# Kernel tuning notes

Hardware: AMD Instinct MI355X
Metric: run time of the kernel (lower is better)

Reference implementation:

```python
import jax, jax.numpy as jnp
import numpy as np

SELECTOR = jnp.array([29, 49, 79])
N_FINAL = 6
N_EM_ITERS = 10
LOG_2PI = float(np.log(2.0 * np.pi))


def _logdet2(c):
    # log determinant of trailing 2x2 matrices
    return jnp.log(c[..., 0, 0] * c[..., 1, 1] - c[..., 0, 1] * c[..., 1, 0])


def _inv2(c):
    # analytic inverse of trailing 2x2 matrices
    det = c[..., 0, 0] * c[..., 1, 1] - c[..., 0, 1] * c[..., 1, 0]
    inv = jnp.stack([
        jnp.stack([c[..., 1, 1], -c[..., 0, 1]], axis=-1),
        jnp.stack([-c[..., 1, 0], c[..., 0, 0]], axis=-1),
    ], axis=-2)
    return inv / det[..., None, None]


def _initial_state(probas, trajectories):
    B, M = probas.shape
    tsel = trajectories[:, :, SELECTOR, :]                       # [B,M,3,2]
    dots = jnp.einsum('bmtd,bntd->btmn', tsel, tsel)             # [B,3,M,M]
    d1 = jnp.einsum('bmtd,bmtd->btm', tsel, tsel)                # [B,3,M]
    R = jnp.sqrt(d1[:, :, :, None] + d1[:, :, None, :] - 2.0 * dots)
    thr = jnp.quantile(R[:, -1].reshape(B, -1), 0.15, axis=-1)[:, None, None, None]
    adj = (R <= thr).astype(probas.dtype).prod(axis=1)           # [B,M,M]
    worked = jnp.ones((B, M), dtype=probas.dtype)
    bidx = jnp.arange(B)
    idxs = []
    for _ in range(N_FINAL):
        score = (adj * probas[:, None, :]).sum(axis=2) * worked  # [B,M]
        amax = jnp.argmax(score, axis=-1)                        # [B]
        worked = worked * (1.0 - adj[bidx, amax])
        idxs.append(amax)
    return jnp.stack(idxs, axis=1)                               # [B,6]


def _coefficients(cov6, trajectories, traj6, probas6):
    cov6_sel = cov6[:, :, SELECTOR]                              # [B,6,3,2,2]
    prec = _inv2(cov6_sel)                                       # [B,6,3,2,2]
    diff = traj6[:, :, SELECTOR][:, :, None] - trajectories[:, :, SELECTOR][:, None]  # [B,6,M,3,2]
    qform = jnp.einsum('bnmti,bntij,bnmtj->bnmt', diff, prec, diff)
    logdet = _logdet2(cov6_sel)[:, :, None, :]                   # [B,6,1,3]
    pM = jnp.exp((-LOG_2PI - 0.5 * logdet - 0.5 * qform).sum(axis=-1)) + 1e-8  # [B,6,M]
    num = pM * probas6[:, :, None]
    return num / (num.sum(axis=1, keepdims=True) + 1e-8)


def _forward(non_normalized_probas, trajectories, covariance_matrices):
    B = trajectories.shape[0]
    probas = jax.nn.softmax(non_normalized_probas, axis=-1)
    idx = jax.lax.stop_gradient(_initial_state(probas, trajectories))  # [B,6]
    b = jnp.arange(B)[:, None]
    traj6 = trajectories[b, idx]                                 # [B,6,T,2]
    probas6 = jax.nn.softmax(jnp.take_along_axis(non_normalized_probas, idx, axis=1), axis=-1)
    cov6 = covariance_matrices[b, idx]                           # [B,6,T,2,2]
    for _ in range(N_EM_ITERS):
        pM = jax.lax.stop_gradient(_coefficients(cov6, trajectories, traj6, probas6))
        P = probas[:, None, :] * pM                              # [B,6,M]
        probas6 = P.sum(axis=-1)                                 # [B,6]
        traj6 = jnp.einsum('bnm,bmtd->bntd', P, trajectories) / probas6[:, :, None, None]
        diff = traj6[:, :, None] - trajectories[:, None]         # [B,6,M,T,2]
        cov6 = (jnp.einsum('bnm,bmtij->bntij', P, covariance_matrices)
                + jnp.einsum('bnm,bnmti,bnmtj->bntij', P, diff, diff)) / probas6[:, :, None, None, None]
    return probas6, traj6, cov6


def setup_inputs() -> dict:
    key = jax.random.key(0)
    k1, k2, k3 = jax.random.split(key, 3)
    B, M, T = 256, 48, 80
    logits = jax.random.normal(k1, (B, M), dtype=jnp.float32)
    trajectories = jax.random.normal(k2, (B, M, T, 2), dtype=jnp.float32)
    A = 0.3 * jax.random.normal(k3, (B, M, T, 2, 2), dtype=jnp.float32)
    cov = A @ jnp.swapaxes(A, -1, -2) + 0.5 * jnp.eye(2, dtype=jnp.float32)
    return {'non_normalized_probas': logits, 'trajectories': trajectories,
            'covariance_matrices': cov}


def reference(non_normalized_probas, trajectories, covariance_matrices):
    return _forward(non_normalized_probas, trajectories, covariance_matrices)
```

## Files before the change

kernel.cpp:

```cpp
#include <hip/hip_runtime.h>
#include <math.h>

#define BATCH 256
#define M 48
#define T 80
#define NF 6
#define EMIT 10
#define MM (M*M)
#define KPL (MM/64)
#define LOG2PI 1.8378770664093453f

typedef unsigned int u32;
typedef unsigned long long u64;

#define WGSYNC()     __asm__ __volatile__("s_waitcnt lgkmcnt(0)\ns_barrier" ::: "memory")
#define WGSYNC_ALL() __asm__ __volatile__("s_waitcnt vmcnt(0) lgkmcnt(0)\ns_barrier" ::: "memory")

__global__ __launch_bounds__(256, 1)
void em_kernel(const float* __restrict__ g_logits,
               const float* __restrict__ g_traj,
               const float* __restrict__ g_cov,
               float* __restrict__ g_out)
{
    const int b = blockIdx.x;
    const int tid = threadIdx.x;
    const int lane = tid & 63;
    const int wv = tid >> 6;
    const int SEL[3] = {29, 49, 79};

    __shared__ __align__(16) float s_txy[M*T*2];
    __shared__ __align__(16) float s_cv4[M*T*4];
    __shared__ float s_adj[MM];
    __shared__ float s_logits[M];
    __shared__ float s_probas[M];
    __shared__ float s_tsel[M*6];
    __shared__ float s_d1[M*3];
    __shared__ __align__(16) float s_csel[M*3*4];
    __shared__ __align__(16) float s_Pm[M*8];
    __shared__ float s_t6sel[2][NF*6];
    __shared__ float s_probas6[2][NF];
    __shared__ float s_prec[2][NF*3*3];
    __shared__ float s_ld[2][NF*3];
    __shared__ int   s_idx[8];
    __shared__ __align__(16) u32 s_hist[4][256];

    const float* traj_b = g_traj + (size_t)b*(M*T*2);
    const float* cov_b  = g_cov  + (size_t)b*(M*T*4);

    float myLogit = -1e30f;
    if (lane < M) myLogit = g_logits[b*M + lane];
    float selx[3], sely[3], cc0[3], cc1[3], cc2[3];
    #pragma unroll
    for (int r = 0; r < 3; ++r) {
        int i = lane + r*64;
        if (i < M*3) {
            int m = i/3, tt = i - (i/3)*3;
            float2 xy = ((const float2*)traj_b)[m*T + SEL[tt]];
            float4 cv = ((const float4*)cov_b)[m*T + SEL[tt]];
            selx[r]=xy.x; sely[r]=xy.y; cc0[r]=cv.x; cc1[r]=cv.y; cc2[r]=cv.w;
        }
    }

    __builtin_amdgcn_sched_barrier(0);
    {
        const char* gt = (const char*)traj_b + lane*16;
        char* lt = (char*)s_txy;
        #pragma unroll 2
        for (int k = wv; k < 30; k += 4)
            __builtin_amdgcn_global_load_lds(
                (const __attribute__((address_space(1))) u32*)(gt + k*1024),
                (__attribute__((address_space(3))) u32*)(lt + k*1024), 16, 0, 0);
        const char* gc = (const char*)cov_b + lane*16;
        char* lc = (char*)s_cv4;
        #pragma unroll 2
        for (int k = wv; k < 60; k += 4)
            __builtin_amdgcn_global_load_lds(
                (const __attribute__((address_space(1))) u32*)(gc + k*1024),
                (__attribute__((address_space(3))) u32*)(lc + k*1024), 16, 0, 0);
    }
    __builtin_amdgcn_sched_barrier(0);

    if (lane < M) s_logits[lane] = myLogit;
    #pragma unroll
    for (int r = 0; r < 3; ++r) {
        int i = lane + r*64;
        if (i < M*3) {
            int m = i/3, tt = i - (i/3)*3;
            s_tsel[m*6+tt*2+0] = selx[r];
            s_tsel[m*6+tt*2+1] = sely[r];
            s_d1[i] = selx[r]*selx[r] + sely[r]*sely[r];
            s_csel[i*4+0]=cc0[r]; s_csel[i*4+1]=cc1[r]; s_csel[i*4+2]=cc2[r]; s_csel[i*4+3]=0.f;
        }
    }

    float mx = myLogit;
    #pragma unroll
    for (int off = 32; off; off >>= 1) mx = fmaxf(mx, __shfl_xor(mx, off));
    float pe = (lane < M) ? __expf(myLogit - mx) : 0.f;
    float psum = pe;
    #pragma unroll
    for (int off = 32; off; off >>= 1) psum += __shfl_xor(psum, off);
    const float proba = pe / psum;
    if (lane < M) s_probas[lane] = proba;

    u32 key[KPL];
    #pragma unroll
    for (int c = 0; c < KPL; ++c) {
        int e = lane + c*64;
        int m = e/M, n = e - (e/M)*M;
        float dot = s_tsel[m*6+4]*s_tsel[n*6+4] + s_tsel[m*6+5]*s_tsel[n*6+5];
        float v = s_d1[m*3+2] + s_d1[n*3+2] - 2.0f*dot;
        key[c] = __float_as_uint(fmaxf(v, 0.0f));
    }

    u32* hist = &s_hist[wv][0];
    int target = 345;
    u32 prefix = 0u, pmask = 0u;
    #pragma unroll 1
    for (int shift = 24; shift >= 0; shift -= 8) {
        ((uint4*)hist)[lane] = make_uint4(0,0,0,0);
        #pragma unroll
        for (int c = 0; c < KPL; ++c) {
            if ((key[c] & pmask) == prefix)
                atomicAdd(&hist[(key[c] >> shift) & 255u], 1u);
        }
        uint4 hv = ((const uint4*)hist)[lane];
        u32 s4 = hv.x + hv.y + hv.z + hv.w;
        u32 cum = s4;
        #pragma unroll
        for (int off = 1; off < 64; off <<= 1) {
            u32 u = __shfl_up(cum, off);
            if (lane >= off) cum += u;
        }
        u64 bmask = __ballot(cum > (u32)target);
        int g = __builtin_ctzll(bmask);
        int dig = 0; u32 binstart = 0;
        if (lane == g) {
            u32 exc = cum - s4;
            int bi2 = lane*4;
            if (exc + hv.x > (u32)target)      { dig = bi2;   binstart = exc; }
            else { exc += hv.x;
                if (exc + hv.y > (u32)target)  { dig = bi2+1; binstart = exc; }
                else { exc += hv.y;
                    if (exc + hv.z > (u32)target) { dig = bi2+2; binstart = exc; }
                    else { exc += hv.z;            dig = bi2+3; binstart = exc; } } }
        }
        dig = __shfl(dig, g);
        binstart = (u32)__shfl((int)binstart, g);
        target -= (int)binstart;
        prefix |= ((u32)dig) << shift;
        pmask  |= (255u << shift);
    }
    const u32 k1 = prefix;
    const float v1f = sqrtf(__uint_as_float(k1));

    float v2f;
    {
        u32 cnt = 0, mng = 0xFFFFFFFFu;
        #pragma unroll
        for (int c = 0; c < KPL; ++c) {
            if (key[c] <= k1) cnt++;
            else mng = (key[c] < mng) ? key[c] : mng;
        }
        #pragma unroll
        for (int off = 32; off > 0; off >>= 1) {
            cnt += __shfl_down(cnt, off);
            u32 mo = (u32)__shfl_down((int)mng, off);
            mng = (mo < mng) ? mo : mng;
        }
        u32 ct = (u32)__shfl((int)cnt, 0);
        u32 mt = (u32)__shfl((int)mng, 0);
        v2f = (ct >= 347u) ? v1f : sqrtf(__uint_as_float(mt));
    }
    const float qi = 0.15f * 2303.0f;
    const float fr = qi - floorf(qi);
    const float thr = v1f*(1.0f - fr) + v2f*fr;

    float dthr;
    {
        u32 ub = __float_as_uint(thr*thr);
        while (sqrtf(__uint_as_float(ub)) > thr) --ub;
        while (sqrtf(__uint_as_float(ub+1u)) <= thr) ++ub;
        dthr = __uint_as_float(ub);
    }

    #pragma unroll
    for (int c = 0; c < KPL; ++c) {
        int e = lane + c*64;
        int m = e/M, n = e - (e/M)*M;
        float d0 = s_tsel[m*6+0]*s_tsel[n*6+0] + s_tsel[m*6+1]*s_tsel[n*6+1];
        float v0 = fmaxf(s_d1[m*3+0] + s_d1[n*3+0] - 2.0f*d0, 0.0f);
        float d1v = s_tsel[m*6+2]*s_tsel[n*6+2] + s_tsel[m*6+3]*s_tsel[n*6+3];
        float v1 = fmaxf(s_d1[m*3+1] + s_d1[n*3+1] - 2.0f*d1v, 0.0f);
        bool a = (__uint_as_float(key[c]) <= dthr) && (v0 <= dthr) && (v1 <= dthr);
        s_adj[e] = a ? 1.0f : 0.0f;
    }

    const int m = (lane < M) ? lane : (M-1);
    {
        float base = 0.f;
        #pragma unroll
        for (int n = 0; n < M; ++n) base += s_adj[n*M+m] * s_probas[n];
        float worked = 1.f;
        #pragma unroll 1
        for (int k = 0; k < NF; ++k) {
            float sc = (lane < M) ? base*worked : -1.f;
            int bi = lane;
            #pragma unroll
            for (int off = 32; off; off >>= 1) {
                float so = __shfl_down(sc, off);
                int io = __shfl_down(bi, off);
                if (so > sc || (so == sc && io < bi)) { sc = so; bi = io; }
            }
            int amax = __shfl(bi, 0);
            if (lane == 0) s_idx[k] = amax;
            worked *= (1.f - s_adj[amax*M+m]);
        }
    }

    if (lane < NF) {
        float mx6 = -1e30f;
        #pragma unroll
        for (int j = 0; j < NF; ++j) mx6 = fmaxf(mx6, s_logits[s_idx[j]]);
        float sum6 = 0.f;
        #pragma unroll
        for (int j = 0; j < NF; ++j) sum6 += __expf(s_logits[s_idx[j]] - mx6);
        s_probas6[0][lane] = __expf(s_logits[s_idx[lane]] - mx6) / sum6;
    }
    if (lane < NF*3) {
        int n = lane/3, tt = lane - (lane/3)*3;
        int m0 = s_idx[n];
        s_t6sel[0][n*6+tt*2+0] = s_tsel[m0*6+tt*2+0];
        s_t6sel[0][n*6+tt*2+1] = s_tsel[m0*6+tt*2+1];
        float c00 = s_csel[(m0*3+tt)*4+0];
        float c01 = s_csel[(m0*3+tt)*4+1];
        float c11 = s_csel[(m0*3+tt)*4+2];
        float det = c00*c11 - c01*c01;
        float rdet = __fdividef(1.0f, det);
        s_prec[0][lane*3+0] =  c11*rdet;
        s_prec[0][lane*3+1] = -c01*rdet;
        s_prec[0][lane*3+2] =  c00*rdet;
        s_ld[0][lane] = __logf(det);
    }

    float tm0=s_tsel[m*6+0], tm1=s_tsel[m*6+1], tm2=s_tsel[m*6+2],
          tm3=s_tsel[m*6+3], tm4=s_tsel[m*6+4], tm5=s_tsel[m*6+5];
    const int gid = tid >> 3;
    const int sub = tid & 7;
    const int gn  = gid/3, gtt = gid - (gid/3)*3;
    const int gslot = (gn < 3) ? gn : gn + 1;

    #pragma unroll 1
    for (int it = 0; it < EMIT; ++it) {
        const int cur = it & 1, nxt = cur ^ 1;
        const float* prC = s_prec[cur];
        const float* ldC = s_ld[cur];
        const float* t6C = s_t6sel[cur];
        const float* p6C = s_probas6[cur];

        float num[NF]; float den = 1e-8f;
        #pragma unroll
        for (int n = 0; n < NF; ++n) {
            float lsum = ldC[n*3+0] + ldC[n*3+1] + ldC[n*3+2];
            float dx0 = t6C[n*6+0]-tm0, dy0 = t6C[n*6+1]-tm1;
            float dx1 = t6C[n*6+2]-tm2, dy1 = t6C[n*6+3]-tm3;
            float dx2 = t6C[n*6+4]-tm4, dy2 = t6C[n*6+5]-tm5;
            float q = prC[(n*3+0)*3+0]*dx0*dx0 + 2.f*prC[(n*3+0)*3+1]*dx0*dy0 + prC[(n*3+0)*3+2]*dy0*dy0
                    + prC[(n*3+1)*3+0]*dx1*dx1 + 2.f*prC[(n*3+1)*3+1]*dx1*dy1 + prC[(n*3+1)*3+2]*dy1*dy1
                    + prC[(n*3+2)*3+0]*dx2*dx2 + 2.f*prC[(n*3+2)*3+1]*dx2*dy2 + prC[(n*3+2)*3+2]*dy2*dy2;
            num[n] = (__expf(-3.f*LOG2PI - 0.5f*lsum - 0.5f*q) + 1e-8f) * p6C[n];
            den += num[n];
        }
        float f = __fdividef(proba, den);
        if (lane < M) {
            *(float4*)&s_Pm[m*8]   = make_float4(num[0]*f, num[1]*f, num[2]*f, 0.f);
            *(float4*)&s_Pm[m*8+4] = make_float4(num[3]*f, num[4]*f, num[5]*f, 0.f);
        }
        if (it == EMIT-1) break;

        if (gid < 18) {
            float SP=0,S1x=0,S1y=0,Sxx=0,Sxy=0,Syy=0,C0=0,C1=0,C2=0;
            #pragma unroll
            for (int k = 0; k < 6; ++k) {
                int mm = sub*6 + k;
                float p = s_Pm[mm*8 + gslot];
                float x = s_tsel[mm*6+gtt*2+0];
                float y = s_tsel[mm*6+gtt*2+1];
                float4 c4 = *(const float4*)&s_csel[(mm*3+gtt)*4];
                SP += p; S1x += p*x; S1y += p*y;
                Sxx += p*x*x; Sxy += p*x*y; Syy += p*y*y;
                C0 += p*c4.x; C1 += p*c4.y; C2 += p*c4.z;
            }
            #define R8(v) { v += __shfl_down(v,4); v += __shfl_down(v,2); v += __shfl_down(v,1); }
            R8(SP) R8(S1x) R8(S1y) R8(Sxx) R8(Sxy) R8(Syy) R8(C0) R8(C1) R8(C2)
            #undef R8
            if (sub == 0) {
                float p6 = SP;
                float tx = __fdividef(S1x, p6), ty = __fdividef(S1y, p6);
                float rp = __fdividef(1.0f, p6);
                float c00 = (C0 + (Sxx - S1x*tx)) * rp;
                float c01 = (C1 + (Sxy - S1x*ty)) * rp;
                float c11 = (C2 + (Syy - S1y*ty)) * rp;
                float det = c00*c11 - c01*c01;
                float rdet = __fdividef(1.0f, det);
                s_prec[nxt][gid*3+0] =  c11*rdet;
                s_prec[nxt][gid*3+1] = -c01*rdet;
                s_prec[nxt][gid*3+2] =  c00*rdet;
                s_ld[nxt][gid] = __logf(det);
                s_t6sel[nxt][gn*6+gtt*2+0] = tx;
                s_t6sel[nxt][gn*6+gtt*2+1] = ty;
                if (gtt == 0) s_probas6[nxt][gn] = SP;
            }
        }
        WGSYNC();
    }

    WGSYNC_ALL();

    float*  out_p = g_out;
    float2* out_t = (float2*)(g_out + BATCH*NF);
    float4* out_c = (float4*)(g_out + BATCH*NF + BATCH*NF*T*2);
    if (lane < 40) {
        int it2 = wv*40 + lane;
        int t = it2 >> 1, half = it2 & 1;
        float SP[3]={0,0,0}, S1x[3]={0,0,0}, S1y[3]={0,0,0};
        float Sxx[3]={0,0,0}, Sxy[3]={0,0,0}, Syy[3]={0,0,0};
        float C00[3]={0,0,0}, C01[3]={0,0,0}, C11[3]={0,0,0};
        #pragma unroll 4
        for (int mm = 0; mm < M; ++mm) {
            float2 xy = ((const float2*)s_txy)[mm*T + t];
            float4 c4 = ((const float4*)s_cv4)[mm*T + t];
            float4 pq = *(const float4*)&s_Pm[mm*8 + half*4];
            float p[3] = {pq.x, pq.y, pq.z};
            float xx = xy.x*xy.x, xyv = xy.x*xy.y, yy = xy.y*xy.y;
            #pragma unroll
            for (int j = 0; j < 3; ++j) {
                SP[j]+=p[j]; S1x[j]+=p[j]*xy.x; S1y[j]+=p[j]*xy.y;
                Sxx[j]+=p[j]*xx; Sxy[j]+=p[j]*xyv; Syy[j]+=p[j]*yy;
                C00[j]+=p[j]*c4.x; C01[j]+=p[j]*c4.y; C11[j]+=p[j]*c4.w;
            }
        }
        #pragma unroll
        for (int j = 0; j < 3; ++j) {
            int n = half*3 + j;
            float p6 = SP[j];
            float tx = __fdividef(S1x[j], p6), ty = __fdividef(S1y[j], p6);
            float rp = __fdividef(1.0f, p6);
            float c00 = (C00[j] + (Sxx[j] - S1x[j]*tx)) * rp;
            float c01 = (C01[j] + (Sxy[j] - S1x[j]*ty)) * rp;
            float c11 = (C11[j] + (Syy[j] - S1y[j]*ty)) * rp;
            size_t o = (size_t)(b*NF + n)*T + t;
            out_t[o] = make_float2(tx, ty);
            out_c[o] = make_float4(c00, c01, c01, c11);
        }
    }
    if (wv == 0 && lane < NF) {
        int slot = (lane < 3) ? lane : lane + 1;
        float sp = 0.f;
        for (int mm = 0; mm < M; ++mm) sp += s_Pm[mm*8 + slot];
        out_p[b*NF + lane] = sp;
    }
}

extern "C" void kernel_launch(void* const* d_in, const int* in_sizes, int n_in,
                              void* d_out, int out_size, void* d_ws, size_t ws_size,
                              hipStream_t stream) {
    const float* logits = (const float*)d_in[0];
    const float* traj   = (const float*)d_in[1];
    const float* cov    = (const float*)d_in[2];
    float* out = (float*)d_out;
    em_kernel<<<dim3(BATCH), dim3(256), 0, stream>>>(logits, traj, cov, out);
}
```

Baseline: 113.0 us.

## Split quantile radix-select across all four waves and rebalance final M-step

The 2304-element pairwise-distance keys used for the quantile threshold were previously computed redundantly by each wave (36 keys per lane). Now each wave takes a quarter of them (9 per lane), builds per-wave histograms for each radix pass, and merges the four histograms through shared memory after a workgroup barrier. The final M-step is also remapped so 60 lanes per wave each handle two mixture components instead of 40 lanes handling three. This cuts redundant ALU and LDS atomic work, at the cost of extra workgroup barriers and cross-wave reductions.

```diff
diff --git a/kernel.cpp b/kernel.cpp
--- a/kernel.cpp
+++ b/kernel.cpp
@@ -7,7 +7,7 @@
 #define NF 6
 #define EMIT 10
 #define MM (M*M)
-#define KPL (MM/64)
+#define KPW 9
 #define LOG2PI 1.8378770664093453f
 
 typedef unsigned int u32;
@@ -42,7 +42,8 @@
     __shared__ float s_prec[2][NF*3*3];
     __shared__ float s_ld[2][NF*3];
     __shared__ int   s_idx[8];
-    __shared__ __align__(16) u32 s_hist[4][256];
+    __shared__ __align__(16) u32 s_hist[4][4][256];
+    __shared__ u32 s_statc[4], s_statm[4];
 
     const float* traj_b = g_traj + (size_t)b*(M*T*2);
     const float* cov_b  = g_cov  + (size_t)b*(M*T*4);
@@ -80,6 +81,12 @@
     }
     __builtin_amdgcn_sched_barrier(0);
 
+    {
+        uint4* hz = (uint4*)&s_hist[wv][0][0];
+        #pragma unroll
+        for (int k = 0; k < 4; ++k) hz[lane + k*64] = make_uint4(0,0,0,0);
+    }
+
     if (lane < M) s_logits[lane] = myLogit;
     #pragma unroll
     for (int r = 0; r < 3; ++r) {
@@ -103,28 +110,40 @@
     const float proba = pe / psum;
     if (lane < M) s_probas[lane] = proba;
 
-    u32 key[KPL];
-    #pragma unroll
-    for (int c = 0; c < KPL; ++c) {
-        int e = lane + c*64;
-        int m = e/M, n = e - (e/M)*M;
-        float dot = s_tsel[m*6+4]*s_tsel[n*6+4] + s_tsel[m*6+5]*s_tsel[n*6+5];
-        float v = s_d1[m*3+2] + s_d1[n*3+2] - 2.0f*dot;
-        key[c] = __float_as_uint(fmaxf(v, 0.0f));
-    }
-
-    u32* hist = &s_hist[wv][0];
+    u32 key[KPW];
+    {
+        u32* h0 = &s_hist[wv][0][0];
+        #pragma unroll
+        for (int j = 0; j < KPW; ++j) {
+            int e = lane + (wv*KPW + j)*64;
+            int m = e/M, n = e - (e/M)*M;
+            float dot = s_tsel[m*6+4]*s_tsel[n*6+4] + s_tsel[m*6+5]*s_tsel[n*6+5];
+            float v = s_d1[m*3+2] + s_d1[n*3+2] - 2.0f*dot;
+            key[j] = __float_as_uint(fmaxf(v, 0.0f));
+            atomicAdd(&h0[key[j] >> 24], 1u);
+        }
+    }
+
     int target = 345;
     u32 prefix = 0u, pmask = 0u;
     #pragma unroll 1
-    for (int shift = 24; shift >= 0; shift -= 8) {
-        ((uint4*)hist)[lane] = make_uint4(0,0,0,0);
-        #pragma unroll
-        for (int c = 0; c < KPL; ++c) {
-            if ((key[c] & pmask) == prefix)
-                atomicAdd(&hist[(key[c] >> shift) & 255u], 1u);
-        }
-        uint4 hv = ((const uint4*)hist)[lane];
+    for (int r = 0; r < 4; ++r) {
+        const int shift = 24 - 8*r;
+        if (r) {
+            u32* hr = &s_hist[wv][r][0];
+            #pragma unroll
+            for (int j = 0; j < KPW; ++j) {
+                if ((key[j] & pmask) == prefix)
+                    atomicAdd(&hr[(key[j] >> shift) & 255u], 1u);
+            }
+        }
+        WGSYNC();
+        uint4 h0 = ((const uint4*)&s_hist[0][r][0])[lane];
+        uint4 h1 = ((const uint4*)&s_hist[1][r][0])[lane];
+        uint4 h2 = ((const uint4*)&s_hist[2][r][0])[lane];
+        uint4 h3 = ((const uint4*)&s_hist[3][r][0])[lane];
+        uint4 hv = make_uint4(h0.x+h1.x+h2.x+h3.x, h0.y+h1.y+h2.y+h3.y,
+                              h0.z+h1.z+h2.z+h3.z, h0.w+h1.w+h2.w+h3.w);
         u32 s4 = hv.x + hv.y + hv.z + hv.w;
         u32 cum = s4;
         #pragma unroll
@@ -154,13 +173,12 @@
     const u32 k1 = prefix;
     const float v1f = sqrtf(__uint_as_float(k1));
 
-    float v2f;
     {
         u32 cnt = 0, mng = 0xFFFFFFFFu;
         #pragma unroll
-        for (int c = 0; c < KPL; ++c) {
-            if (key[c] <= k1) cnt++;
-            else mng = (key[c] < mng) ? key[c] : mng;
+        for (int j = 0; j < KPW; ++j) {
+            if (key[j] <= k1) cnt++;
+            else mng = (key[j] < mng) ? key[j] : mng;
         }
         #pragma unroll
         for (int off = 32; off > 0; off >>= 1) {
@@ -168,8 +186,16 @@
             u32 mo = (u32)__shfl_down((int)mng, off);
             mng = (mo < mng) ? mo : mng;
         }
-        u32 ct = (u32)__shfl((int)cnt, 0);
-        u32 mt = (u32)__shfl((int)mng, 0);
+        if (lane == 0) { s_statc[wv] = cnt; s_statm[wv] = mng; }
+    }
+    WGSYNC();
+    float v2f;
+    {
+        u32 ct = s_statc[0]+s_statc[1]+s_statc[2]+s_statc[3];
+        u32 mt = s_statm[0];
+        if (s_statm[1] < mt) mt = s_statm[1];
+        if (s_statm[2] < mt) mt = s_statm[2];
+        if (s_statm[3] < mt) mt = s_statm[3];
         v2f = (ct >= 347u) ? v1f : sqrtf(__uint_as_float(mt));
     }
     const float qi = 0.15f * 2303.0f;
@@ -185,16 +211,17 @@
     }
 
     #pragma unroll
-    for (int c = 0; c < KPL; ++c) {
-        int e = lane + c*64;
+    for (int j = 0; j < KPW; ++j) {
+        int e = lane + (wv*KPW + j)*64;
         int m = e/M, n = e - (e/M)*M;
         float d0 = s_tsel[m*6+0]*s_tsel[n*6+0] + s_tsel[m*6+1]*s_tsel[n*6+1];
         float v0 = fmaxf(s_d1[m*3+0] + s_d1[n*3+0] - 2.0f*d0, 0.0f);
         float d1v = s_tsel[m*6+2]*s_tsel[n*6+2] + s_tsel[m*6+3]*s_tsel[n*6+3];
         float v1 = fmaxf(s_d1[m*3+1] + s_d1[n*3+1] - 2.0f*d1v, 0.0f);
-        bool a = (__uint_as_float(key[c]) <= dthr) && (v0 <= dthr) && (v1 <= dthr);
+        bool a = (__uint_as_float(key[j]) <= dthr) && (v0 <= dthr) && (v1 <= dthr);
         s_adj[e] = a ? 1.0f : 0.0f;
     }
+    WGSYNC();
 
     const int m = (lane < M) ? lane : (M-1);
     {
@@ -320,36 +347,47 @@
     float*  out_p = g_out;
     float2* out_t = (float2*)(g_out + BATCH*NF);
     float4* out_c = (float4*)(g_out + BATCH*NF + BATCH*NF*T*2);
-    if (lane < 40) {
-        int it2 = wv*40 + lane;
-        int t = it2 >> 1, half = it2 & 1;
-        float SP[3]={0,0,0}, S1x[3]={0,0,0}, S1y[3]={0,0,0};
-        float Sxx[3]={0,0,0}, Sxy[3]={0,0,0}, Syy[3]={0,0,0};
-        float C00[3]={0,0,0}, C01[3]={0,0,0}, C11[3]={0,0,0};
+    if (lane < 60) {
+        int idx = wv*60 + lane;
+        int t = idx/3, third = idx - (idx/3)*3;
+        int nA = third*2, nB = nA + 1;
+        int slotA = (nA < 3) ? nA : nA + 1;
+        int slotB = (nB < 3) ? nB : nB + 1;
+        float SPa=0,S1xa=0,S1ya=0,Sxxa=0,Sxya=0,Syya=0,C00a=0,C01a=0,C11a=0;
+        float SPb=0,S1xb=0,S1yb=0,Sxxb=0,Sxyb=0,Syyb=0,C00b=0,C01b=0,C11b=0;
         #pragma unroll 4
         for (int mm = 0; mm < M; ++mm) {
             float2 xy = ((const float2*)s_txy)[mm*T + t];
             float4 c4 = ((const float4*)s_cv4)[mm*T + t];
-            float4 pq = *(const float4*)&s_Pm[mm*8 + half*4];
-            float p[3] = {pq.x, pq.y, pq.z};
+            float pa = s_Pm[mm*8 + slotA];
+            float pb = s_Pm[mm*8 + slotB];
             float xx = xy.x*xy.x, xyv = xy.x*xy.y, yy = xy.y*xy.y;
-            #pragma unroll
-            for (int j = 0; j < 3; ++j) {
-                SP[j]+=p[j]; S1x[j]+=p[j]*xy.x; S1y[j]+=p[j]*xy.y;
-                Sxx[j]+=p[j]*xx; Sxy[j]+=p[j]*xyv; Syy[j]+=p[j]*yy;
-                C00[j]+=p[j]*c4.x; C01[j]+=p[j]*c4.y; C11[j]+=p[j]*c4.w;
-            }
-        }
-        #pragma unroll
-        for (int j = 0; j < 3; ++j) {
-            int n = half*3 + j;
-            float p6 = SP[j];
-            float tx = __fdividef(S1x[j], p6), ty = __fdividef(S1y[j], p6);
+            SPa+=pa; S1xa+=pa*xy.x; S1ya+=pa*xy.y;
+            Sxxa+=pa*xx; Sxya+=pa*xyv; Syya+=pa*yy;
+            C00a+=pa*c4.x; C01a+=pa*c4.y; C11a+=pa*c4.w;
+            SPb+=pb; S1xb+=pb*xy.x; S1yb+=pb*xy.y;
+            Sxxb+=pb*xx; Sxyb+=pb*xyv; Syyb+=pb*yy;
+            C00b+=pb*c4.x; C01b+=pb*c4.y; C11b+=pb*c4.w;
+        }
+        {
+            float p6 = SPa;
+            float tx = __fdividef(S1xa, p6), ty = __fdividef(S1ya, p6);
             float rp = __fdividef(1.0f, p6);
-            float c00 = (C00[j] + (Sxx[j] - S1x[j]*tx)) * rp;
-            float c01 = (C01[j] + (Sxy[j] - S1x[j]*ty)) * rp;
-            float c11 = (C11[j] + (Syy[j] - S1y[j]*ty)) * rp;
-            size_t o = (size_t)(b*NF + n)*T + t;
+            float c00 = (C00a + (Sxxa - S1xa*tx)) * rp;
+            float c01 = (C01a + (Sxya - S1xa*ty)) * rp;
+            float c11 = (C11a + (Syya - S1ya*ty)) * rp;
+            size_t o = (size_t)(b*NF + nA)*T + t;
+            out_t[o] = make_float2(tx, ty);
+            out_c[o] = make_float4(c00, c01, c01, c11);
+        }
+        {
+            float p6 = SPb;
+            float tx = __fdividef(S1xb, p6), ty = __fdividef(S1yb, p6);
+            float rp = __fdividef(1.0f, p6);
+            float c00 = (C00b + (Sxxb - S1xb*tx)) * rp;
+            float c01 = (C01b + (Sxyb - S1xb*ty)) * rp;
+            float c11 = (C11b + (Syyb - S1yb*ty)) * rp;
+            size_t o = (size_t)(b*NF + nB)*T + t;
             out_t[o] = make_float2(tx, ty);
             out_c[o] = make_float4(c00, c01, c01, c11);
         }
```

Result: faster. 105.4 us (-6.7%).
